# Kernel tuning notes

Measured on AMD Instinct MI355X. Metric: run time of the kernel, lower is better.

Reference implementation:

```python
import jax, jax.numpy as jnp
import numpy as np
from jax import lax

DIM = 256
HEADS = 8
DIM_HEAD = 64
INNER = HEADS * DIM_HEAD  # 512
K = 3
PAD = K // 2
KV_STRIDE = 2
SCALE = DIM_HEAD ** -0.5
BN_EPS = 1e-5


def _dw_block(x, w_dw, g, b, m, v, w_pw, stride):
    """depthwise conv -> batchnorm (eval) -> 1x1 conv. x: [B,C,H,W]."""
    c = x.shape[1]
    h = lax.conv_general_dilated(
        x, w_dw, window_strides=(stride, stride),
        padding=[(PAD, PAD), (PAD, PAD)],
        feature_group_count=c,
        dimension_numbers=('NCHW', 'OIHW', 'NCHW'))
    inv = lax.rsqrt(v + BN_EPS)
    h = (h - m[None, :, None, None]) * (g * inv)[None, :, None, None] + b[None, :, None, None]
    return jnp.einsum('oc,bchw->bohw', w_pw, h)


def _heads_flat(t):
    # [B, h*d, H, W] -> [B, h, d, H*W]
    B, hd, H, W = t.shape
    return t.reshape(B, HEADS, DIM_HEAD, H * W)


def _cross_attn(q, k, v, Hq, Wq):
    # q: [B,h,d,i], k/v: [B,h,d,j]
    dots = jnp.einsum('bhdi,bhdj->bhij', q, k) * SCALE
    attn = jax.nn.softmax(dots, axis=-1)
    out = jnp.einsum('bhij,bhdj->bhdi', attn, v)
    B = q.shape[0]
    return out.reshape(B, INNER, Hq, Wq)


def _forward(x, y, q_dw_w, q_bn_gamma, q_bn_beta, q_bn_mean, q_bn_var, q_pw_w,
             kv_dw_w, kv_bn_gamma, kv_bn_beta, kv_bn_mean, kv_bn_var, kv_pw_w,
             out_w, out_b):
    B, _, Hx, Wx = x.shape
    _, _, Hy, Wy = y.shape

    qx = _heads_flat(_dw_block(x, q_dw_w, q_bn_gamma, q_bn_beta, q_bn_mean, q_bn_var, q_pw_w, 1))
    kvx = _dw_block(x, kv_dw_w, kv_bn_gamma, kv_bn_beta, kv_bn_mean, kv_bn_var, kv_pw_w, KV_STRIDE)
    kx, vx = map(_heads_flat, jnp.split(kvx, 2, axis=1))

    qy = _heads_flat(_dw_block(y, q_dw_w, q_bn_gamma, q_bn_beta, q_bn_mean, q_bn_var, q_pw_w, 1))
    kvy = _dw_block(y, kv_dw_w, kv_bn_gamma, kv_bn_beta, kv_bn_mean, kv_bn_var, kv_pw_w, KV_STRIDE)
    ky, vy = map(_heads_flat, jnp.split(kvy, 2, axis=1))

    outx = _cross_attn(qx, ky, vy, Hx, Wx)   # x queries attend to y keys/values
    outy = _cross_attn(qy, kx, vx, Hy, Wy)   # y queries attend to x keys/values

    def proj(o):
        return jnp.einsum('oc,bchw->bohw', out_w, o) + out_b[None, :, None, None]

    return proj(outx), proj(outy)


def setup_inputs() -> dict:
    key = jax.random.key(0)
    ks = jax.random.split(key, 8)
    B, H, W = 8, 32, 32
    return {
        'x': jax.random.normal(ks[0], (B, DIM, H, W), jnp.float32),
        'y': jax.random.normal(ks[1], (B, DIM, H, W), jnp.float32),
        'q_dw_w': jax.random.normal(ks[2], (DIM, 1, K, K), jnp.float32) * 0.1,
        'q_bn_gamma': jnp.ones((DIM,), jnp.float32),
        'q_bn_beta': jnp.zeros((DIM,), jnp.float32),
        'q_bn_mean': jnp.zeros((DIM,), jnp.float32),
        'q_bn_var': jnp.ones((DIM,), jnp.float32),
        'q_pw_w': jax.random.normal(ks[3], (INNER, DIM), jnp.float32) * (DIM ** -0.5),
        'kv_dw_w': jax.random.normal(ks[4], (DIM, 1, K, K), jnp.float32) * 0.1,
        'kv_bn_gamma': jnp.ones((DIM,), jnp.float32),
        'kv_bn_beta': jnp.zeros((DIM,), jnp.float32),
        'kv_bn_mean': jnp.zeros((DIM,), jnp.float32),
        'kv_bn_var': jnp.ones((DIM,), jnp.float32),
        'kv_pw_w': jax.random.normal(ks[5], (2 * INNER, DIM), jnp.float32) * (DIM ** -0.5),
        'out_w': jax.random.normal(ks[6], (DIM, INNER), jnp.float32) * (INNER ** -0.5),
        'out_b': jnp.zeros((DIM,), jnp.float32),
    }


def reference(x, y, q_dw_w, q_bn_gamma, q_bn_beta, q_bn_mean, q_bn_var, q_pw_w,
              kv_dw_w, kv_bn_gamma, kv_bn_beta, kv_bn_mean, kv_bn_var, kv_pw_w,
              out_w, out_b):
    return _forward(x, y, q_dw_w, q_bn_gamma, q_bn_beta, q_bn_mean, q_bn_var, q_pw_w,
                    kv_dw_w, kv_bn_gamma, kv_bn_beta, kv_bn_mean, kv_bn_var, kv_pw_w,
                    out_w, out_b)
```

## Files before the change

### kernel.cpp

```cpp
#include <hip/hip_runtime.h>

#define BN_EPS 1e-5f
#define ATT_SCALE 0.125f

typedef _Float16 half_t;
typedef _Float16 half8 __attribute__((ext_vector_type(8)));
typedef _Float16 half4 __attribute__((ext_vector_type(4)));
typedef float f32x4 __attribute__((ext_vector_type(4)));

__device__ __forceinline__ void gll16(const void* g, void* l) {
    __builtin_amdgcn_global_load_lds((const __attribute__((address_space(1))) void*)g,
                                     (__attribute__((address_space(3))) void*)l, 16, 0, 0);
}

template<int N>
__device__ __forceinline__ void vmwait() {
    asm volatile("s_waitcnt vmcnt(%0)" :: "i"(N) : "memory");
}

__device__ void prep_body(
    int o, int c,
    const float* qg, const float* qb, const float* qm, const float* qv, const float* qpw,
    const float* kg, const float* kbt, const float* km, const float* kvv, const float* kvpw,
    const float* outw,
    half_t* wq, half_t* wkv, half_t* wout, float* bq, float* bkv, float* red)
{
    if (o >= 1536) {
        int ro = o - 1536;
        #pragma unroll
        for (int ci = 0; ci < 2; ++ci) {
            int cc = ci * 256 + c;
            float wv = outw[(size_t)ro * 512 + cc];
            half_t hh = (half_t)wv;
            wout[(size_t)ro * 1024 + cc]       = hh;
            wout[(size_t)ro * 1024 + 512 + cc] = (half_t)(wv - (float)hh);
        }
        return;
    }
    const float *g, *b, *m, *v, *w; half_t* we; float* be;
    if (o < 512) {
        g = qg; b = qb; m = qm; v = qv;
        w = qpw + (size_t)o * 256; we = wq + (size_t)o * 512; be = bq + o;
    } else {
        int ro = o - 512;
        g = kg; b = kbt; m = km; v = kvv;
        w = kvpw + (size_t)ro * 256; we = wkv + (size_t)ro * 512; be = bkv + ro;
    }
    float s  = g[c] * rsqrtf(v[c] + BN_EPS);
    float tt = b[c] - m[c] * s;
    float wv = w[c];
    float wsv = wv * s;
    half_t hh = (half_t)wsv;
    we[c]       = hh;
    we[256 + c] = (half_t)(wsv - (float)hh);
    float partial = wv * tt;
    #pragma unroll
    for (int off = 32; off > 0; off >>= 1)
        partial += __shfl_down(partial, off, 64);
    if ((c & 63) == 0) red[c >> 6] = partial;
    __syncthreads();
    if (c == 0) *be = red[0] + red[1] + red[2] + red[3];
}

__device__ void dw_body(
    int rp, int img, float* sin,
    const float* x, const float* y,
    const float* qdw, const float* kvdw,
    half_t* qB, half_t* kvB)
{
    const float* in = (img < 8) ? x + (size_t)img * 256 * 1024
                                : y + (size_t)(img - 8) * 256 * 1024;
    int t = threadIdx.x;
    int ch = t & 63, cg = t >> 6;
    int r0 = 2 * rp - 1;
    #pragma unroll
    for (int u = t; u < 1024; u += 256) {
        int c = u >> 4, row = (u >> 2) & 3, pi = u & 3;
        sin[c * 148 + row * 36 + (pi < 2 ? pi : 32 + pi)] = 0.f;
    }
    for (int cc = 0; cc < 4; ++cc) {
        __syncthreads();
        #pragma unroll
        for (int ii = 0; ii < 8; ++ii) {
            int u = ii * 256 + t;
            int sch = u >> 5, row = (u >> 3) & 3, seg = u & 7;
            int gr = r0 + row;
            float4 v4 = {0.f, 0.f, 0.f, 0.f};
            if (gr >= 0 && gr < 32)
                v4 = *(const float4*)(in + (size_t)(cc * 64 + sch) * 1024 + gr * 32 + seg * 4);
            float* d = &sin[sch * 148 + row * 36 + 2 + seg * 4];
            d[0] = v4.x; d[1] = v4.y; d[2] = v4.z; d[3] = v4.w;
        }
        __syncthreads();
        int gch = cc * 64 + ch;
        float wq9[9], wk9[9];
        #pragma unroll
        for (int i = 0; i < 9; ++i) { wq9[i] = qdw[gch * 9 + i]; wk9[i] = kvdw[gch * 9 + i]; }
        float rowv[4][12];
        const float* base = &sin[ch * 148];
        #pragma unroll
        for (int rr = 0; rr < 4; ++rr) {
            *(float4*)&rowv[rr][0] = *(const float4*)(base + rr * 36 + cg * 8);
            *(float4*)&rowv[rr][4] = *(const float4*)(base + rr * 36 + cg * 8 + 4);
            *(float4*)&rowv[rr][8] = *(const float4*)(base + rr * 36 + cg * 8 + 8);
        }
        #pragma unroll
        for (int r = 0; r < 2; ++r) {
            #pragma unroll
            for (int c8 = 0; c8 < 8; ++c8) {
                float acc = 0.f;
                #pragma unroll
                for (int dr = 0; dr < 3; ++dr)
                    #pragma unroll
                    for (int dc = 0; dc < 3; ++dc)
                        acc += wq9[dr * 3 + dc] * rowv[r + dr][c8 + dc + 1];
                half_t hh = (half_t)acc;
                size_t p = (size_t)img * 1024 + (2 * rp + r) * 32 + cg * 8 + c8;
                qB[p * 512 + gch]       = hh;
                qB[p * 512 + 256 + gch] = (half_t)(acc - (float)hh);
            }
        }
        #pragma unroll
        for (int c4 = 0; c4 < 4; ++c4) {
            float acc = 0.f;
            #pragma unroll
            for (int dr = 0; dr < 3; ++dr)
                #pragma unroll
                for (int dc = 0; dc < 3; ++dc)
                    acc += wk9[dr * 3 + dc] * rowv[dr][2 * c4 + dc + 1];
            half_t hh = (half_t)acc;
            size_t p = (size_t)img * 256 + rp * 16 + cg * 4 + c4;
            kvB[p * 512 + gch]       = hh;
            kvB[p * 512 + 256 + gch] = (half_t)(acc - (float)hh);
        }
    }
}

__global__ __launch_bounds__(256) void prep_dw_kernel(
    const float* __restrict__ x, const float* __restrict__ y,
    const float* __restrict__ qdw, const float* __restrict__ kvdw,
    const float* __restrict__ qg, const float* __restrict__ qb,
    const float* __restrict__ qm, const float* __restrict__ qv,
    const float* __restrict__ qpw,
    const float* __restrict__ kg, const float* __restrict__ kbt,
    const float* __restrict__ km, const float* __restrict__ kvv,
    const float* __restrict__ kvpw,
    const float* __restrict__ outw,
    half_t* __restrict__ wq, half_t* __restrict__ wkv, half_t* __restrict__ wout,
    float* __restrict__ bq, float* __restrict__ bkv,
    half_t* __restrict__ qB, half_t* __restrict__ kvB)
{
    __shared__ __align__(16) float smem[64 * 148];
    int bx = blockIdx.x;
    if (bx < 256)
        dw_body(bx & 15, bx >> 4, smem, x, y, qdw, kvdw, qB, kvB);
    else
        prep_body(bx - 256, threadIdx.x, qg, qb, qm, qv, qpw,
                  kg, kbt, km, kvv, kvpw, outw, wq, wkv, wout, bq, bkv, smem);
}

template<int MT, int NT, int WGM, int WGN, int NTHR, int MODE, int KTOT>
__device__ __forceinline__ void gemm_worker(
    char* lds, const half_t* Ab, const half_t* Bb,
    void* outBuf, const float* bias,
    int NPX, int img, int m0, int n0, float scale)
{
    constexpr int TM = WGM * MT * 16, TN = WGN * NT * 16;
    constexpr int BUF = (TM + TN) * 128;
    constexpr int NC = KTOT / 32;
    constexpr int GCNT = 8 * (TM + TN) / NTHR;
    int t = threadIdx.x, w = t >> 6, lane = t & 63, quad = lane >> 4, l15 = lane & 15;
    int wm = w % WGM, wn = w / WGM;
    f32x4 acc[MT][NT] = {};

    auto stage = [&](int kh, int p) {
        char* Ah = lds + p * BUF;
        char* Al = Ah + TM * 64;
        char* Bh = Ah + TM * 128;
        char* Bl = Bh + TN * 64;
        #pragma unroll
        for (int ii = 0; ii < TM * 4 / NTHR; ++ii) {
            int u = ii * NTHR + t;
            int mt = u >> 6, q = (u >> 4) & 3, r = u & 15;
            const half_t* g = Ab + (size_t)(mt * 16 + r) * (2 * KTOT) + kh + q * 8;
            gll16(g,        Ah + (u & ~63) * 16);
            gll16(g + KTOT, Al + (u & ~63) * 16);
        }
        #pragma unroll
        for (int ii = 0; ii < TN * 4 / NTHR; ++ii) {
            int u = ii * NTHR + t;
            int nt = u >> 6, q = (u >> 4) & 3, r = u & 15;
            const half_t* g = Bb + (size_t)(nt * 16 + r) * (2 * KTOT) + kh + q * 8;
            gll16(g,        Bh + (u & ~63) * 16);
            gll16(g + KTOT, Bl + (u & ~63) * 16);
        }
    };

    stage(0, 0);
    for (int kc = 0; kc < NC; ++kc) {
        if (kc + 1 < NC) { stage((kc + 1) * 32, (kc + 1) & 1); vmwait<GCNT>(); }
        else             { vmwait<0>(); }
        __builtin_amdgcn_s_barrier();
        __builtin_amdgcn_sched_barrier(0);
        char* Ah = lds + (kc & 1) * BUF;
        char* Al = Ah + TM * 64;
        char* Bh = Ah + TM * 128;
        char* Bl = Bh + TN * 64;
        half8 afh[MT], afl[MT];
        #pragma unroll
        for (int mi = 0; mi < MT; ++mi) {
            afh[mi] = *(half8*)(Ah + (wm * MT + mi) * 1024 + lane * 16);
            afl[mi] = *(half8*)(Al + (wm * MT + mi) * 1024 + lane * 16);
        }
        __builtin_amdgcn_s_setprio(1);
        #pragma unroll
        for (int ni = 0; ni < NT; ++ni) {
            half8 bh = *(half8*)(Bh + (wn * NT + ni) * 1024 + lane * 16);
            half8 bl = *(half8*)(Bl + (wn * NT + ni) * 1024 + lane * 16);
            #pragma unroll
            for (int mi = 0; mi < MT; ++mi) {
                acc[mi][ni] = __builtin_amdgcn_mfma_f32_16x16x32_f16(afh[mi], bh, acc[mi][ni], 0, 0, 0);
                acc[mi][ni] = __builtin_amdgcn_mfma_f32_16x16x32_f16(afh[mi], bl, acc[mi][ni], 0, 0, 0);
                acc[mi][ni] = __builtin_amdgcn_mfma_f32_16x16x32_f16(afl[mi], bh, acc[mi][ni], 0, 0, 0);
            }
        }
        __builtin_amdgcn_s_setprio(0);
        __builtin_amdgcn_s_barrier();
        __builtin_amdgcn_sched_barrier(0);
    }

    if (MODE == 2) {
        #pragma unroll
        for (int mi = 0; mi < MT; ++mi) {
            int mrow0 = m0 + wm * MT * 16 + mi * 16 + quad * 4;
            #pragma unroll
            for (int ni = 0; ni < NT; ++ni) {
                int col = n0 + wn * NT * 16 + ni * 16 + l15;
                f32x4 a = acc[mi][ni];
                float* op = (float*)outBuf + (size_t)img * 256 * NPX;
                #pragma unroll
                for (int r = 0; r < 4; ++r)
                    op[(size_t)(mrow0 + r) * NPX + col] = a[r] + bias[mrow0 + r];
            }
        }
    } else {
        __syncthreads();
        float* tbuf = (float*)lds;
        constexpr int TP = 40;
        #pragma unroll
        for (int qtr = 0; qtr < TM / 32; ++qtr) {
            #pragma unroll
            for (int mi = 0; mi < MT; ++mi) {
                int rowblk = wm * MT * 16 + mi * 16;
                if (rowblk >= qtr * 32 && rowblk < qtr * 32 + 32) {
                    int mloc = rowblk - qtr * 32 + quad * 4;
                    #pragma unroll
                    for (int ni = 0; ni < NT; ++ni) {
                        int nloc = wn * NT * 16 + ni * 16 + l15;
                        #pragma unroll
                        for (int r = 0; r < 4; ++r) {
                            float vv = acc[mi][ni][r];
                            if (MODE == 0) vv = (vv + bias[m0 + rowblk + quad * 4 + r]) * scale;
                            else           vv = vv + bias[n0 + nloc];
                            tbuf[nloc * TP + mloc + r] = vv;
                        }
                    }
                }
            }
            __syncthreads();
            #pragma unroll
            for (int it = 0; it < (TN * 4) / NTHR; ++it) {
                int u = it * NTHR + t;
                int n = u >> 2, mg = u & 3;
                float vv[8];
                *(float4*)&vv[0] = *(const float4*)&tbuf[n * TP + mg * 8];
                *(float4*)&vv[4] = *(const float4*)&tbuf[n * TP + mg * 8 + 4];
                half8 hv, lv;
                #pragma unroll
                for (int j = 0; j < 8; ++j) {
                    half_t hh = (half_t)vv[j];
                    hv[j] = hh; lv[j] = (half_t)(vv[j] - (float)hh);
                }
                int mglob = m0 + qtr * 32 + mg * 8;
                if (MODE == 0) {
                    int h = mglob >> 6, d0 = mglob & 63;
                    half_t* op = (half_t*)outBuf + ((size_t)(img * 8 + h) * NPX + n0 + n) * 128 + d0;
                    *(half8*)op = hv;
                    *(half8*)(op + 64) = lv;
                } else {
                    int nn = n0 + n, h = nn >> 6, d = nn & 63;
                    int j0 = mglob;
                    half_t* op = (half_t*)outBuf + (size_t)(img * 8 + h) * 32768
                               + (j0 >> 5) * 4096 + ((d >> 4) & 3) * 512 + ((j0 >> 4) & 1) * 256
                               + ((j0 >> 2) & 3) * 64 + (d & 15) * 4;
                    half4 a0 = {hv[0], hv[1], hv[2], hv[3]};
                    half4 a1 = {hv[4], hv[5], hv[6], hv[7]};
                    half4 b0 = {lv[0], lv[1], lv[2], lv[3]};
                    half4 b1 = {lv[4], lv[5], lv[6], lv[7]};
                    *(half4*)op               = a0;
                    *(half4*)(op + 64)        = a1;
                    *(half4*)(op + 2048)      = b0;
                    *(half4*)(op + 2048 + 64) = b1;
                }
            }
            __syncthreads();
        }
    }
}

__global__ __launch_bounds__(512, 4) void qkv_kernel(
    const half_t* __restrict__ wq, const half_t* __restrict__ wkv,
    const half_t* __restrict__ qB, const half_t* __restrict__ kvB,
    const float* __restrict__ bq, const float* __restrict__ bkv,
    half_t* __restrict__ qpr, half_t* __restrict__ kpr, half_t* __restrict__ vpr)
{
    __shared__ __align__(16) char lds[65536];
    int tile = blockIdx.x, img = blockIdx.z;
    if (tile < 32) {
        int m0 = (tile >> 3) * 128, n0 = (tile & 7) * 128;
        gemm_worker<2, 4, 4, 2, 512, 0, 256>(lds,
            wq + (size_t)m0 * 512,
            qB + (size_t)img * (1024 * 512) + (size_t)n0 * 512,
            qpr, bq, 1024, img, m0, n0, ATT_SCALE);
    } else if (tile < 40) {
        int tt = tile - 32;
        int m0 = (tt >> 1) * 128, n0 = (tt & 1) * 128;
        gemm_worker<2, 4, 4, 2, 512, 0, 256>(lds,
            wkv + (size_t)m0 * 512,
            kvB + (size_t)img * (256 * 512) + (size_t)n0 * 512,
            kpr, bkv, 256, img, m0, n0, 1.0f);
    } else {
        int tt = tile - 40;
        int m0 = (tt >> 2) * 128, n0 = (tt & 3) * 128;
        gemm_worker<2, 4, 4, 2, 512, 1, 256>(lds,
            kvB + (size_t)img * (256 * 512) + (size_t)m0 * 512,
            wkv + (size_t)(512 + n0) * 512,
            vpr, bkv + 512, 512, img, m0, n0, 1.0f);
    }
}

__global__ __launch_bounds__(256, 3) void out_kernel(
    const half_t* __restrict__ wout, const half_t* __restrict__ attp,
    const float* __restrict__ outb, float* __restrict__ out)
{
    __shared__ __align__(16) char lds[49152];
    int tile = blockIdx.x, img = blockIdx.z;
    int m0 = (tile >> 3) * 64, n0 = (tile & 7) * 128;
    gemm_worker<2, 4, 2, 2, 256, 2, 512>(lds,
        wout + (size_t)m0 * 1024,
        attp + (size_t)img * (1024 * 1024) + (size_t)n0 * 1024,
        out, outb, 1024, img, m0, n0, 1.0f);
}

__global__ __launch_bounds__(512, 4) void attn_fused(
    const half_t* __restrict__ qb, const half_t* __restrict__ kb,
    const half_t* __restrict__ vb, half_t* __restrict__ att)
{
    __shared__ __align__(16) char lds[33792];
    int ic = blockIdx.y;
    int img = blockIdx.x & 15, h = blockIdx.x >> 4;
    int partner = img ^ 8;
    int t = threadIdx.x, w = t >> 6, lane = t & 63, quad = lane >> 4, l15 = lane & 15;
    const half_t* qp = qb + ((size_t)(img * 8 + h) * 1024 + ic * 128) * 128;
    const half_t* kp = kb + (size_t)(partner * 8 + h) * 256 * 128;
    const half_t* vp = vb + (size_t)(partner * 8 + h) * 32768;

    half8 qh[2], ql[2];
    #pragma unroll
    for (int kcs = 0; kcs < 2; ++kcs) {
        const half_t* qr = qp + (size_t)(w * 16 + l15) * 128 + kcs * 32 + quad * 8;
        qh[kcs] = *(const half8*)qr;
        ql[kcs] = *(const half8*)(qr + 64);
    }

    auto stageC = [&](int c) {
        char* buf = lds + (c & 3) * 8192;
        if (c < 8) {
            int sb = t >> 6, li = t & 63;
            int plane = sb >> 2, ntr = (sb >> 1) & 1, kcs = sb & 1;
            const half_t* g = kp + (size_t)(c * 32 + ntr * 16 + (li & 15)) * 128
                                 + plane * 64 + kcs * 32 + (li >> 4) * 8;
            gll16(g, buf + (t & ~63) * 16);
        } else {
            gll16(vp + (size_t)(c - 8) * 4096 + t * 8, buf + (t & ~63) * 16);
        }
    };

    f32x4 sacc[16] = {};
    f32x4 oacc[4] = {};
    float mx = 0.f, lsum = 0.f;

    stageC(0); stageC(1); stageC(2);

    #pragma unroll
    for (int c = 0; c < 16; ++c) {
        if (c < 14)       vmwait<2>();
        else if (c == 14) vmwait<1>();
        else              vmwait<0>();
        __builtin_amdgcn_s_barrier();
        __builtin_amdgcn_sched_barrier(0);
        if (c + 3 < 16) stageC(c + 3);
        const char* buf = lds + (c & 3) * 8192;
        if (c < 8) {
            __builtin_amdgcn_s_setprio(1);
            #pragma unroll
            for (int kcs = 0; kcs < 2; ++kcs)
                #pragma unroll
                for (int ntr = 0; ntr < 2; ++ntr) {
                    half8 kh = *(const half8*)(buf + (ntr * 2 + kcs) * 1024 + lane * 16);
                    half8 kl = *(const half8*)(buf + 4096 + (ntr * 2 + kcs) * 1024 + lane * 16);
                    f32x4 s = sacc[c * 2 + ntr];
                    s = __builtin_amdgcn_mfma_f32_16x16x32_f16(kh, qh[kcs], s, 0, 0, 0);
                    s = __builtin_amdgcn_mfma_f32_16x16x32_f16(kh, ql[kcs], s, 0, 0, 0);
                    s = __builtin_amdgcn_mfma_f32_16x16x32_f16(kl, qh[kcs], s, 0, 0, 0);
                    sacc[c * 2 + ntr] = s;
                }
            __builtin_amdgcn_s_setprio(0);
        } else {
            if (c == 8) {
                float m_ = sacc[0][0];
                #pragma unroll
                for (int ti = 0; ti < 16; ++ti)
                    #pragma unroll
                    for (int r = 0; r < 4; ++r) m_ = fmaxf(m_, sacc[ti][r]);
                m_ = fmaxf(m_, __shfl_xor(m_, 16, 64));
                mx = fmaxf(m_, __shfl_xor(m_, 32, 64));
            }
            int jc = c - 8;
            half4 pb[2][2];
            #pragma unroll
            for (int kk = 0; kk < 2; ++kk) {
                f32x4 s = sacc[jc * 2 + kk];
                #pragma unroll
                for (int e = 0; e < 4; ++e) {
                    float pv = __expf(s[e] - mx);
                    lsum += pv;
                    half_t hh = (half_t)pv;
                    pb[kk][0][e] = hh;
                    pb[kk][1][e] = (half_t)(pv - (float)hh);
                }
            }
            __builtin_amdgcn_s_setprio(1);
            #pragma unroll
            for (int mt = 0; mt < 4; ++mt) {
                #pragma unroll
                for (int kk = 0; kk < 2; ++kk) {
                    half4 vh = *(const half4*)(buf + (mt * 2 + kk) * 512 + lane * 8);
                    half4 vl = *(const half4*)(buf + 4096 + (mt * 2 + kk) * 512 + lane * 8);
                    f32x4 o = oacc[mt];
                    o = __builtin_amdgcn_mfma_f32_16x16x16f16(vh, pb[kk][0], o, 0, 0, 0);
                    o = __builtin_amdgcn_mfma_f32_16x16x16f16(vh, pb[kk][1], o, 0, 0, 0);
                    o = __builtin_amdgcn_mfma_f32_16x16x16f16(vl, pb[kk][0], o, 0, 0, 0);
                    oacc[mt] = o;
                }
            }
            __builtin_amdgcn_s_setprio(0);
        }
    }

    lsum += __shfl_xor(lsum, 16, 64);
    lsum += __shfl_xor(lsum, 32, 64);
    float inv = 1.f / lsum;

    __syncthreads();
    #pragma unroll
    for (int mt = 0; mt < 4; ++mt)
        #pragma unroll
        for (int r = 0; r < 4; ++r) {
            float vv = oacc[mt][r] * inv;
            half_t hh = (half_t)vv;
            int row = w * 16 + l15;
            int d = mt * 16 + quad * 4 + r;
            *(half_t*)(lds + (row * 132 + d) * 2)      = hh;
            *(half_t*)(lds + (row * 132 + 64 + d) * 2) = (half_t)(vv - (float)hh);
        }
    __syncthreads();
    #pragma unroll
    for (int ii = 0; ii < 4; ++ii) {
        int u = ii * 512 + t;
        int i = u >> 4, seg = (u >> 3) & 1, p8 = u & 7;
        half8 val = *(const half8*)(lds + (i * 132 + seg * 64 + p8 * 8) * 2);
        *(half8*)(att + ((size_t)img * 1024 + ic * 128 + i) * 1024
                  + seg * 512 + h * 64 + p8 * 8) = val;
    }
}

extern "C" void kernel_launch(void* const* d_in, const int* in_sizes, int n_in,
                              void* d_out, int out_size, void* d_ws, size_t ws_size,
                              hipStream_t stream) {
    const float* x    = (const float*)d_in[0];
    const float* y    = (const float*)d_in[1];
    const float* qdw  = (const float*)d_in[2];
    const float* qg   = (const float*)d_in[3];
    const float* qbb  = (const float*)d_in[4];
    const float* qm   = (const float*)d_in[5];
    const float* qv   = (const float*)d_in[6];
    const float* qpw  = (const float*)d_in[7];
    const float* kvdw = (const float*)d_in[8];
    const float* kg   = (const float*)d_in[9];
    const float* kb_  = (const float*)d_in[10];
    const float* km   = (const float*)d_in[11];
    const float* kvv  = (const float*)d_in[12];
    const float* kvpw = (const float*)d_in[13];
    const float* outw = (const float*)d_in[14];
    const float* outb = (const float*)d_in[15];

    char* ws = (char*)d_ws;
    half_t* wq   = (half_t*)(ws);
    half_t* wkv  = (half_t*)(ws + 524288);
    half_t* wout = (half_t*)(ws + 1572864);
    float*  bq   = (float*) (ws + 2097152);
    float*  bkv  = (float*) (ws + 2099200);
    half_t* qpr  = (half_t*)(ws + 2103296);
    half_t* kpr  = (half_t*)(ws + 35657728);
    half_t* vpr  = (half_t*)(ws + 44046336);
    half_t* qB   = (half_t*)(ws + 52434944);
    half_t* kvB  = (half_t*)(ws + 69212160);
    half_t* attp = (half_t*)(ws + 52434944);

    prep_dw_kernel<<<2048, 256, 0, stream>>>(
        x, y, qdw, kvdw, qg, qbb, qm, qv, qpw, kg, kb_, km, kvv, kvpw, outw,
        wq, wkv, wout, bq, bkv, qB, kvB);

    qkv_kernel<<<dim3(48, 1, 16), 512, 0, stream>>>(
        wq, wkv, qB, kvB, bq, bkv, qpr, kpr, vpr);

    attn_fused<<<dim3(128, 8, 1), 512, 0, stream>>>(qpr, kpr, vpr, attp);

    out_kernel<<<dim3(32, 1, 16), 256, 0, stream>>>(wout, attp, outb, (float*)d_out);
}
```

Baseline: 204.0 us.

## Load low-half fp16 operands directly to registers, halve LDS staging in GEMMs

The split-fp16 GEMM worker now stages only the high halves of A and B through LDS via global_load_lds. The low halves are loaded straight from global memory into registers, double-buffered one k-chunk ahead. Tiles change to 128x128 with 4 waves of 4x4 MFMA blocks, and out_kernel uses larger 128-row tiles with half the blocks. This halves LDS traffic and footprint, at the cost of uncoalesced per-lane global loads, more registers and lower occupancy (launch bounds 256,2).

Measured after the change: 242.6 us. 18.9% more time.

```diff
diff --git a/kernel.cpp b/kernel.cpp
--- a/kernel.cpp
+++ b/kernel.cpp
@@ -159,83 +159,91 @@
                   kg, kbt, km, kvv, kvpw, outw, wq, wkv, wout, bq, bkv, smem);
 }
 
-template<int MT, int NT, int WGM, int WGN, int NTHR, int MODE, int KTOT>
-__device__ __forceinline__ void gemm_worker(
-    char* lds, const half_t* Ab, const half_t* Bb,
-    void* outBuf, const float* bias,
-    int NPX, int img, int m0, int n0, float scale)
-{
-    constexpr int TM = WGM * MT * 16, TN = WGN * NT * 16;
-    constexpr int BUF = (TM + TN) * 128;
+template<int MODE, int KTOT>
+__device__ void gemm_w2(char* lds, const half_t* Ab, const half_t* Bb,
+                        void* outBuf, const float* bias,
+                        int NPX, int img, int m0, int n0, float scale)
+{
     constexpr int NC = KTOT / 32;
-    constexpr int GCNT = 8 * (TM + TN) / NTHR;
     int t = threadIdx.x, w = t >> 6, lane = t & 63, quad = lane >> 4, l15 = lane & 15;
-    int wm = w % WGM, wn = w / WGM;
-    f32x4 acc[MT][NT] = {};
+    int wm = w & 1, wn = w >> 1;
+    f32x4 acc[4][4] = {};
 
     auto stage = [&](int kh, int p) {
-        char* Ah = lds + p * BUF;
-        char* Al = Ah + TM * 64;
-        char* Bh = Ah + TM * 128;
-        char* Bl = Bh + TN * 64;
-        #pragma unroll
-        for (int ii = 0; ii < TM * 4 / NTHR; ++ii) {
-            int u = ii * NTHR + t;
+        char* Ah = lds + p * 16384;
+        char* Bh = Ah + 8192;
+        #pragma unroll
+        for (int ii = 0; ii < 2; ++ii) {
+            int u = ii * 256 + t;
             int mt = u >> 6, q = (u >> 4) & 3, r = u & 15;
-            const half_t* g = Ab + (size_t)(mt * 16 + r) * (2 * KTOT) + kh + q * 8;
-            gll16(g,        Ah + (u & ~63) * 16);
-            gll16(g + KTOT, Al + (u & ~63) * 16);
-        }
-        #pragma unroll
-        for (int ii = 0; ii < TN * 4 / NTHR; ++ii) {
-            int u = ii * NTHR + t;
+            gll16(Ab + (size_t)(mt * 16 + r) * (2 * KTOT) + kh + q * 8, Ah + (u & ~63) * 16);
+        }
+        #pragma unroll
+        for (int ii = 0; ii < 2; ++ii) {
+            int u = ii * 256 + t;
             int nt = u >> 6, q = (u >> 4) & 3, r = u & 15;
-            const half_t* g = Bb + (size_t)(nt * 16 + r) * (2 * KTOT) + kh + q * 8;
-            gll16(g,        Bh + (u & ~63) * 16);
-            gll16(g + KTOT, Bl + (u & ~63) * 16);
+            gll16(Bb + (size_t)(nt * 16 + r) * (2 * KTOT) + kh + q * 8, Bh + (u & ~63) * 16);
         }
     };
-
+    auto loadLo = [&](int kh, half8* alo, half8* blo) {
+        #pragma unroll
+        for (int mi = 0; mi < 4; ++mi)
+            alo[mi] = *(const half8*)(Ab + (size_t)((wm * 4 + mi) * 16 + l15) * (2 * KTOT)
+                                      + KTOT + kh + quad * 8);
+        #pragma unroll
+        for (int ni = 0; ni < 4; ++ni)
+            blo[ni] = *(const half8*)(Bb + (size_t)((wn * 4 + ni) * 16 + l15) * (2 * KTOT)
+                                      + KTOT + kh + quad * 8);
+    };
+    auto compute = [&](int p, half8* alo, half8* blo) {
+        char* Ah = lds + p * 16384;
+        char* Bh = Ah + 8192;
+        half8 afh[4];
+        #pragma unroll
+        for (int mi = 0; mi < 4; ++mi)
+            afh[mi] = *(const half8*)(Ah + (wm * 4 + mi) * 1024 + lane * 16);
+        __builtin_amdgcn_s_setprio(1);
+        #pragma unroll
+        for (int ni = 0; ni < 4; ++ni) {
+            half8 bh = *(const half8*)(Bh + (wn * 4 + ni) * 1024 + lane * 16);
+            #pragma unroll
+            for (int mi = 0; mi < 4; ++mi) {
+                acc[mi][ni] = __builtin_amdgcn_mfma_f32_16x16x32_f16(afh[mi], bh,      acc[mi][ni], 0, 0, 0);
+                acc[mi][ni] = __builtin_amdgcn_mfma_f32_16x16x32_f16(afh[mi], blo[ni], acc[mi][ni], 0, 0, 0);
+                acc[mi][ni] = __builtin_amdgcn_mfma_f32_16x16x32_f16(alo[mi], bh,      acc[mi][ni], 0, 0, 0);
+            }
+        }
+        __builtin_amdgcn_s_setprio(0);
+    };
+
+    half8 aloA[4], bloA[4], aloB[4], bloB[4];
     stage(0, 0);
+    loadLo(0, aloA, bloA);
+    #pragma unroll
     for (int kc = 0; kc < NC; ++kc) {
-        if (kc + 1 < NC) { stage((kc + 1) * 32, (kc + 1) & 1); vmwait<GCNT>(); }
-        else             { vmwait<0>(); }
+        if (kc + 1 < NC) {
+            stage((kc + 1) * 32, (kc + 1) & 1);
+            if (kc & 1) loadLo((kc + 1) * 32, aloA, bloA);
+            else        loadLo((kc + 1) * 32, aloB, bloB);
+            vmwait<12>();
+        } else {
+            vmwait<0>();
+        }
         __builtin_amdgcn_s_barrier();
         __builtin_amdgcn_sched_barrier(0);
-        char* Ah = lds + (kc & 1) * BUF;
-        char* Al = Ah + TM * 64;
-        char* Bh = Ah + TM * 128;
-        char* Bl = Bh + TN * 64;
-        half8 afh[MT], afl[MT];
-        #pragma unroll
-        for (int mi = 0; mi < MT; ++mi) {
-            afh[mi] = *(half8*)(Ah + (wm * MT + mi) * 1024 + lane * 16);
-            afl[mi] = *(half8*)(Al + (wm * MT + mi) * 1024 + lane * 16);
-        }
-        __builtin_amdgcn_s_setprio(1);
-        #pragma unroll
-        for (int ni = 0; ni < NT; ++ni) {
-            half8 bh = *(half8*)(Bh + (wn * NT + ni) * 1024 + lane * 16);
-            half8 bl = *(half8*)(Bl + (wn * NT + ni) * 1024 + lane * 16);
-            #pragma unroll
-            for (int mi = 0; mi < MT; ++mi) {
-                acc[mi][ni] = __builtin_amdgcn_mfma_f32_16x16x32_f16(afh[mi], bh, acc[mi][ni], 0, 0, 0);
-                acc[mi][ni] = __builtin_amdgcn_mfma_f32_16x16x32_f16(afh[mi], bl, acc[mi][ni], 0, 0, 0);
-                acc[mi][ni] = __builtin_amdgcn_mfma_f32_16x16x32_f16(afl[mi], bh, acc[mi][ni], 0, 0, 0);
-            }
-        }
-        __builtin_amdgcn_s_setprio(0);
+        if (kc & 1) compute(kc & 1, aloB, bloB);
+        else        compute(kc & 1, aloA, bloA);
         __builtin_amdgcn_s_barrier();
         __builtin_amdgcn_sched_barrier(0);
     }
 
     if (MODE == 2) {
         #pragma unroll
-        for (int mi = 0; mi < MT; ++mi) {
-            int mrow0 = m0 + wm * MT * 16 + mi * 16 + quad * 4;
-            #pragma unroll
-            for (int ni = 0; ni < NT; ++ni) {
-                int col = n0 + wn * NT * 16 + ni * 16 + l15;
+        for (int mi = 0; mi < 4; ++mi) {
+            int mrow0 = m0 + wm * 64 + mi * 16 + quad * 4;
+            #pragma unroll
+            for (int ni = 0; ni < 4; ++ni) {
+                int col = n0 + wn * 64 + ni * 16 + l15;
                 f32x4 a = acc[mi][ni];
                 float* op = (float*)outBuf + (size_t)img * 256 * NPX;
                 #pragma unroll
@@ -248,29 +256,29 @@
         float* tbuf = (float*)lds;
         constexpr int TP = 40;
         #pragma unroll
-        for (int qtr = 0; qtr < TM / 32; ++qtr) {
-            #pragma unroll
-            for (int mi = 0; mi < MT; ++mi) {
-                int rowblk = wm * MT * 16 + mi * 16;
-                if (rowblk >= qtr * 32 && rowblk < qtr * 32 + 32) {
-                    int mloc = rowblk - qtr * 32 + quad * 4;
+        for (int qtr = 0; qtr < 4; ++qtr) {
+            if (wm == (qtr >> 1)) {
+                #pragma unroll
+                for (int mi2 = 0; mi2 < 2; ++mi2) {
+                    int mi = (qtr & 1) * 2 + mi2;
                     #pragma unroll
-                    for (int ni = 0; ni < NT; ++ni) {
-                        int nloc = wn * NT * 16 + ni * 16 + l15;
+                    for (int ni = 0; ni < 4; ++ni) {
+                        int nloc = wn * 64 + ni * 16 + l15;
                         #pragma unroll
                         for (int r = 0; r < 4; ++r) {
                             float vv = acc[mi][ni][r];
-                            if (MODE == 0) vv = (vv + bias[m0 + rowblk + quad * 4 + r]) * scale;
+                            int mloc = mi2 * 16 + quad * 4 + r;
+                            if (MODE == 0) vv = (vv + bias[m0 + qtr * 32 + mloc]) * scale;
                             else           vv = vv + bias[n0 + nloc];
-                            tbuf[nloc * TP + mloc + r] = vv;
+                            tbuf[nloc * TP + mloc] = vv;
                         }
                     }
                 }
             }
             __syncthreads();
             #pragma unroll
-            for (int it = 0; it < (TN * 4) / NTHR; ++it) {
-                int u = it * NTHR + t;
+            for (int it = 0; it < 2; ++it) {
+                int u = it * 256 + t;
                 int n = u >> 2, mg = u & 3;
                 float vv[8];
                 *(float4*)&vv[0] = *(const float4*)&tbuf[n * TP + mg * 8];
@@ -308,45 +316,45 @@
     }
 }
 
-__global__ __launch_bounds__(512, 4) void qkv_kernel(
+__global__ __launch_bounds__(256, 2) void qkv_kernel(
     const half_t* __restrict__ wq, const half_t* __restrict__ wkv,
     const half_t* __restrict__ qB, const half_t* __restrict__ kvB,
     const float* __restrict__ bq, const float* __restrict__ bkv,
     half_t* __restrict__ qpr, half_t* __restrict__ kpr, half_t* __restrict__ vpr)
 {
-    __shared__ __align__(16) char lds[65536];
+    __shared__ __align__(16) char lds[32768];
     int tile = blockIdx.x, img = blockIdx.z;
     if (tile < 32) {
         int m0 = (tile >> 3) * 128, n0 = (tile & 7) * 128;
-        gemm_worker<2, 4, 4, 2, 512, 0, 256>(lds,
+        gemm_w2<0, 256>(lds,
             wq + (size_t)m0 * 512,
             qB + (size_t)img * (1024 * 512) + (size_t)n0 * 512,
             qpr, bq, 1024, img, m0, n0, ATT_SCALE);
     } else if (tile < 40) {
         int tt = tile - 32;
         int m0 = (tt >> 1) * 128, n0 = (tt & 1) * 128;
-        gemm_worker<2, 4, 4, 2, 512, 0, 256>(lds,
+        gemm_w2<0, 256>(lds,
             wkv + (size_t)m0 * 512,
             kvB + (size_t)img * (256 * 512) + (size_t)n0 * 512,
             kpr, bkv, 256, img, m0, n0, 1.0f);
     } else {
         int tt = tile - 40;
         int m0 = (tt >> 2) * 128, n0 = (tt & 3) * 128;
-        gemm_worker<2, 4, 4, 2, 512, 1, 256>(lds,
+        gemm_w2<1, 256>(lds,
             kvB + (size_t)img * (256 * 512) + (size_t)m0 * 512,
             wkv + (size_t)(512 + n0) * 512,
             vpr, bkv + 512, 512, img, m0, n0, 1.0f);
     }
 }
 
-__global__ __launch_bounds__(256, 3) void out_kernel(
+__global__ __launch_bounds__(256, 2) void out_kernel(
     const half_t* __restrict__ wout, const half_t* __restrict__ attp,
     const float* __restrict__ outb, float* __restrict__ out)
 {
-    __shared__ __align__(16) char lds[49152];
+    __shared__ __align__(16) char lds[32768];
     int tile = blockIdx.x, img = blockIdx.z;
-    int m0 = (tile >> 3) * 64, n0 = (tile & 7) * 128;
-    gemm_worker<2, 4, 2, 2, 256, 2, 512>(lds,
+    int m0 = (tile >> 3) * 128, n0 = (tile & 7) * 128;
+    gemm_w2<2, 512>(lds,
         wout + (size_t)m0 * 1024,
         attp + (size_t)img * (1024 * 1024) + (size_t)n0 * 1024,
         out, outb, 1024, img, m0, n0, 1.0f);
@@ -522,10 +530,10 @@
         x, y, qdw, kvdw, qg, qbb, qm, qv, qpw, kg, kb_, km, kvv, kvpw, outw,
         wq, wkv, wout, bq, bkv, qB, kvB);
 
-    qkv_kernel<<<dim3(48, 1, 16), 512, 0, stream>>>(
+    qkv_kernel<<<dim3(48, 1, 16), 256, 0, stream>>>(
         wq, wkv, qB, kvB, bq, bkv, qpr, kpr, vpr);
 
     attn_fused<<<dim3(128, 8, 1), 512, 0, stream>>>(qpr, kpr, vpr, attp);
 
-    out_kernel<<<dim3(32, 1, 16), 256, 0, stream>>>(wout, attp, outb, (float*)d_out);
-}
+    out_kernel<<<dim3(16, 1, 16), 256, 0, stream>>>(wout, attp, outb, (float*)d_out);
+}
```
